# Performance work log

Hardware: AMD Instinct MI355X
Metric: run time of the kernel (lower is better)

Reference implementation:

```python
import jax, jax.numpy as jnp
import numpy as np

IMG_H, IMG_W = 512.0, 512.0
PRE_NMS = 2000   # training-mode pre_nms_top_n
POST_NMS = 2000  # training-mode post_nms_top_n
NMS_THRESH = 0.7
SCORE_THRESH = 0.0
MIN_SIZE = 0.001


def setup_inputs() -> dict:
    key = jax.random.key(0)
    k1, k2, k3 = jax.random.split(key, 3)
    N = 8
    num_anchors_per_level = (49152, 12288, 3072, 768, 192)  # strides 4..64, 3 anchors/loc on 512^2
    A = sum(num_anchors_per_level)
    cxy = jax.random.uniform(k1, (N, A, 2), minval=0.0, maxval=512.0)
    wh = jax.random.uniform(k2, (N, A, 2), minval=2.0, maxval=120.0)
    proposals = jnp.concatenate([cxy - wh / 2, cxy + wh / 2], axis=-1)  # xyxy
    objectness = jax.random.normal(k3, (N, A), dtype=jnp.float32)
    return {"proposals": proposals, "objectness": objectness,
            "num_anchors_per_level": num_anchors_per_level}


def _box_iou(a, b):
    # a: [K,4], b: [K,4] -> [K,K] pairwise IoU (torchvision box_iou semantics)
    area_a = (a[:, 2] - a[:, 0]) * (a[:, 3] - a[:, 1])
    area_b = (b[:, 2] - b[:, 0]) * (b[:, 3] - b[:, 1])
    lt = jnp.maximum(a[:, None, :2], b[None, :, :2])
    rb = jnp.minimum(a[:, None, 2:], b[None, :, 2:])
    wh = jnp.clip(rb - lt, 0.0)
    inter = wh[..., 0] * wh[..., 1]
    return inter / (area_a[:, None] + area_b[None, :] - inter)


def _per_image(boxes, scores, lvl):
    # boxes [K,4] xyxy, scores [K] (sigmoid probs), lvl [K] int32 level ids
    # 1) clip to image
    x = jnp.clip(boxes[:, 0::2], 0.0, IMG_W)
    y = jnp.clip(boxes[:, 1::2], 0.0, IMG_H)
    boxes = jnp.stack([x[:, 0], y[:, 0], x[:, 1], y[:, 1]], axis=-1)
    # 2) small-box + 3) score-threshold masks (masking instead of boolean indexing)
    ws = boxes[:, 2] - boxes[:, 0]
    hs = boxes[:, 3] - boxes[:, 1]
    valid = (ws >= MIN_SIZE) & (hs >= MIN_SIZE) & (scores >= SCORE_THRESH)
    # 4) batched NMS: offset boxes per level so levels never overlap
    off = lvl.astype(boxes.dtype) * (jnp.max(boxes) + 1.0)
    off_boxes = boxes + off[:, None]
    sm = jnp.where(valid, scores, -jnp.inf)
    order = jnp.argsort(-sm)                 # descending score, invalid last
    boxes_s = boxes[order]
    scores_s = scores[order]
    valid_s = valid[order]
    ob_s = jax.lax.stop_gradient(off_boxes[order])
    K = ob_s.shape[0]
    iou = _box_iou(ob_s, ob_s)               # [K,K], keep decision is non-differentiable
    j = jnp.arange(K)
    def body(i, keep):
        suppress = keep[i] & (iou[i] > NMS_THRESH) & (j > i)
        return keep & ~suppress
    keep = jax.lax.fori_loop(0, K, body, valid_s)
    # 5) top post_nms kept boxes, padded to fixed size with zeros
    rank = jnp.cumsum(keep.astype(jnp.int32)) - 1
    sel_key = jnp.where(keep & (rank < POST_NMS), rank, K)
    idx = jnp.argsort(sel_key)[:POST_NMS]
    out_valid = sel_key[idx] < K
    out_boxes = jnp.where(out_valid[:, None], boxes_s[idx], 0.0)
    out_scores = jnp.where(out_valid, scores_s[idx], 0.0)
    return out_boxes, out_scores


def _forward(proposals, objectness, num_anchors_per_level):
    N = proposals.shape[0]
    napl = [int(n) for n in num_anchors_per_level]
    # per-level, per-image top-k on objectness (get_top_n_idx)
    idx_list, lv_list, off = [], [], 0
    for i, n in enumerate(napl):
        k = min(PRE_NMS, n)
        _, ti = jax.lax.top_k(objectness[:, off:off + n], k)
        idx_list.append(ti + off)
        lv_list.append(jnp.full((k,), i, dtype=jnp.int32))
        off += n
    top_idx = jnp.concatenate(idx_list, axis=1)   # [N, K_total]
    lvls = jnp.concatenate(lv_list)               # [K_total], same for every image
    bidx = jnp.arange(N)[:, None]
    obj = objectness[bidx, top_idx]
    props = proposals[bidx, top_idx]
    scores = jax.nn.sigmoid(obj)
    return jax.vmap(lambda b, s: _per_image(b, s, lvls))(props, scores)


def reference(proposals, objectness, num_anchors_per_level):
    # returns (boxes [N, POST_NMS, 4], scores [N, POST_NMS]); invalid slots zero-padded
    return _forward(proposals, objectness, num_anchors_per_level)
```

## Files before the change

kernel.cpp:

```cpp
#include <hip/hip_runtime.h>
#include <math.h>

#define NIMG 8
#define ATOT 65472
#define KTOT 6960
#define POST 2000
#define TILES_PER_IMG 1668
#define NTILES (NIMG*TILES_PER_IMG)
#define ESEG 1024
#define M_TIE 0.7000000178813934326171875
#define PAD(i) ((i) + ((i) >> 5))
#define WAVE_SYNC() asm volatile("s_waitcnt lgkmcnt(0)" ::: "memory")

__constant__ int c_NAPL[5]  = {49152,12288,3072,768,192};
__constant__ int c_LOFF[5]  = {0,49152,61440,64512,65280};
__constant__ int c_KSEL[5]  = {2000,2000,2000,768,192};
__constant__ int c_CBASE[5] = {0,2000,4000,6000,6768};
__constant__ int c_GLVL[5]  = {32,32,32,12,3};
__constant__ int c_TILEPFX[6] = {0,528,1056,1584,1662,1668};

__device__ __forceinline__ unsigned f2u(float f){
  unsigned b = __float_as_uint(f);
  return (b & 0x80000000u) ? ~b : (b | 0x80000000u);
}
__device__ __forceinline__ unsigned long long mkkey(unsigned u, unsigned gidx){
  return ((unsigned long long)u << 32) | (unsigned long long)(0xFFFFFFFFu - gidx);
}
__device__ __forceinline__ unsigned long long shflx64(unsigned long long v, int m){
  int lo = __shfl_xor((int)(unsigned)v, m);
  int hi = __shfl_xor((int)(unsigned)(v >> 32), m);
  return ((unsigned long long)(unsigned)hi << 32) | (unsigned)lo;
}
__device__ __forceinline__ unsigned long long bstep(unsigned long long v, int elem,
                                                    int size, int st){
  unsigned long long p = shflx64(v, st);
  bool lower = (elem & st) == 0;
  bool desc  = (elem & size) == 0;
  bool takeMax = (lower == desc);
  bool gt = v > p;
  return (takeMax == gt) ? v : p;
}

extern "C" __global__ void __launch_bounds__(1024)
k_select(const float* __restrict__ prop, const float* __restrict__ obj,
         unsigned long long* __restrict__ cand, float4* __restrict__ cbox,
         unsigned* __restrict__ zzone){
  __shared__ unsigned long long sb[2112];
  __shared__ unsigned hist[4096];
  __shared__ unsigned scan[1024];
  __shared__ unsigned h8[256];
  __shared__ unsigned s_b12, s_cumAbove, s_t20, s_cnt;
  int task = blockIdx.x, img = task/5, lvl = task%5;
  int n = c_NAPL[lvl], k = c_KSEL[lvl], tid = threadIdx.x;
  if (task == 0)
    for (int i = tid; i < 1280; i += 1024) zzone[i] = 0u;

  const float4* o4 = (const float4*)(obj + (size_t)img*ATOT + c_LOFF[lvl]);
  int n4 = n >> 2;
  unsigned kk = (unsigned)k;
  unsigned T = 0u;
  if (k < n){
    for (int i = tid; i < 4096; i += 1024) hist[i] = 0u;
    if (tid < 256) h8[tid] = 0u;
    __syncthreads();
    for (int i = tid; i < n4; i += 1024){
      float4 v = o4[i];
      atomicAdd(&hist[f2u(v.x) >> 20], 1u);
      atomicAdd(&hist[f2u(v.y) >> 20], 1u);
      atomicAdd(&hist[f2u(v.z) >> 20], 1u);
      atomicAdd(&hist[f2u(v.w) >> 20], 1u);
    }
    __syncthreads();
    unsigned own[4]; unsigned s = 0;
    int b0 = tid*4;
    #pragma unroll
    for (int j = 0; j < 4; ++j){ own[j] = hist[b0+j]; s += own[j]; }
    scan[tid] = s;
    __syncthreads();
    for (int d = 1; d < 1024; d <<= 1){
      unsigned v = (tid + d < 1024) ? scan[tid + d] : 0u;
      __syncthreads();
      scan[tid] += v;
      __syncthreads();
    }
    {
      unsigned R = scan[tid] - s;
      unsigned sufn = R;
      #pragma unroll
      for (int j = 3; j >= 0; --j){
        unsigned sufj = sufn + own[j];
        if (sufj >= kk && sufn < kk){ s_b12 = (unsigned)(b0 + j); s_cumAbove = sufn; }
        sufn = sufj;
      }
    }
    __syncthreads();
    unsigned b12 = s_b12;
    for (int i = tid; i < n4; i += 1024){
      float4 v = o4[i];
      unsigned ux = f2u(v.x), uy = f2u(v.y), uz = f2u(v.z), uw = f2u(v.w);
      if ((ux >> 20) == b12) atomicAdd(&h8[(ux >> 12) & 255u], 1u);
      if ((uy >> 20) == b12) atomicAdd(&h8[(uy >> 12) & 255u], 1u);
      if ((uz >> 20) == b12) atomicAdd(&h8[(uz >> 12) & 255u], 1u);
      if ((uw >> 20) == b12) atomicAdd(&h8[(uw >> 12) & 255u], 1u);
    }
    __syncthreads();
    if (tid < 256) scan[tid] = h8[tid];
    __syncthreads();
    for (int d = 1; d < 256; d <<= 1){
      unsigned v = 0;
      if (tid < 256) v = (tid + d < 256) ? scan[tid + d] : 0u;
      __syncthreads();
      if (tid < 256) scan[tid] += v;
      __syncthreads();
    }
    if (tid < 256){
      unsigned sufj = s_cumAbove + scan[tid];
      unsigned sufn = s_cumAbove + ((tid < 255) ? scan[tid + 1] : 0u);
      if (sufj >= kk && sufn < kk) s_t20 = (s_b12 << 8) | (unsigned)tid;
    }
    __syncthreads();
    T = s_t20;
  }
  if (tid == 0) s_cnt = 0u;
  __syncthreads();
  int abase = c_LOFF[lvl];
  int lane = tid & 63, wv = tid >> 6;
  for (int i = tid; i < n4; i += 1024){
    float4 v = o4[i];
    float vv[4] = {v.x, v.y, v.z, v.w};
    #pragma unroll
    for (int c2 = 0; c2 < 4; ++c2){
      unsigned u = f2u(vv[c2]);
      bool pred = (u >> 12) >= T;
      unsigned long long bm = __ballot(pred);
      unsigned cw = (unsigned)__popcll(bm);
      unsigned basep = 0;
      if (lane == 0 && cw) basep = atomicAdd(&s_cnt, cw);
      basep = __shfl(basep, 0);
      if (pred){
        unsigned p = basep + (unsigned)__popcll(bm & ((1ull << lane) - 1ull));
        if (p < 2048u) sb[PAD(p)] = mkkey(u, (unsigned)(abase + i*4 + c2));
      }
    }
  }
  __syncthreads();
  int cnt = (int)min(s_cnt, 2048u);
  int m = 256; while (m < k || m < cnt) m <<= 1;
  for (int i = cnt + tid; i < m; i += 1024) sb[PAD(i)] = 0ull;
  __syncthreads();

  int elemA = (wv << 7) | lane, elemB = elemA | 64;
  bool active = (elemA < m);
  unsigned long long va = 0ull, vb = 0ull;
  if (active){ va = sb[PAD(elemA)]; vb = sb[PAD(elemB)]; }
  if (active){
    for (int size = 2; size <= 64; size <<= 1)
      for (int st = size >> 1; st >= 1; st >>= 1){
        va = bstep(va, elemA, size, st);
        vb = bstep(vb, elemB, size, st);
      }
    {
      bool desc = ((elemA & 128) == 0);
      unsigned long long mx = (va > vb) ? va : vb;
      unsigned long long mn = (va > vb) ? vb : va;
      va = desc ? mx : mn; vb = desc ? mn : mx;
      for (int st = 32; st >= 1; st >>= 1){
        va = bstep(va, elemA, 128, st);
        vb = bstep(vb, elemB, 128, st);
      }
    }
  }
  for (int S = 256; S <= m; S <<= 1){
    if (active){ sb[PAD(elemA)] = va; sb[PAD(elemB)] = vb; }
    __syncthreads();
    for (int st = S >> 1; st >= 128; st >>= 1){
      for (int t = tid; t < (m >> 1); t += 1024){
        int lo = t & (st - 1);
        int i  = ((t - lo) << 1) + lo;
        int j  = i + st;
        bool desc = ((i & S) == 0);
        unsigned long long x = sb[PAD(i)], y = sb[PAD(j)];
        if (desc ? (x < y) : (x > y)){ sb[PAD(i)] = y; sb[PAD(j)] = x; }
      }
      __syncthreads();
    }
    if (active){
      va = sb[PAD(elemA)]; vb = sb[PAD(elemB)];
      bool desc = ((elemA & S) == 0);
      unsigned long long mx = (va > vb) ? va : vb;
      unsigned long long mn = (va > vb) ? vb : va;
      va = desc ? mx : mn; vb = desc ? mn : mx;
      for (int st = 32; st >= 1; st >>= 1){
        va = bstep(va, elemA, S, st);
        vb = bstep(vb, elemB, S, st);
      }
    }
  }
  const float4* pr = (const float4*)(prop + (size_t)img*ATOT*4);
  size_t base = (size_t)img*KTOT + c_CBASE[lvl];
  if (active){
    if (elemA < k){
      cand[base + elemA] = va;
      unsigned gidx = 0xFFFFFFFFu - (unsigned)(va & 0xFFFFFFFFull);
      float4 p = pr[gidx];
      cbox[base + elemA] = make_float4(fminf(fmaxf(p.x,0.f),512.f), fminf(fmaxf(p.y,0.f),512.f),
                                       fminf(fmaxf(p.z,0.f),512.f), fminf(fmaxf(p.w,0.f),512.f));
    }
    if (elemB < k){
      cand[base + elemB] = vb;
      unsigned gidx = 0xFFFFFFFFu - (unsigned)(vb & 0xFFFFFFFFull);
      float4 p = pr[gidx];
      cbox[base + elemB] = make_float4(fminf(fmaxf(p.x,0.f),512.f), fminf(fmaxf(p.y,0.f),512.f),
                                       fminf(fmaxf(p.z,0.f),512.f), fminf(fmaxf(p.w,0.f),512.f));
    }
  }
}

extern "C" __global__ void __launch_bounds__(256)
k_mask(const float4* __restrict__ cbox, unsigned* __restrict__ ecnt,
       unsigned* __restrict__ eseg, float4* __restrict__ out4, int out_n4){
  __shared__ float4 colb[4][64];
  __shared__ float  colA[4][64];
  int tid = threadIdx.x, lane = tid & 63, wv = tid >> 6;
  int bid = blockIdx.x;
  if (bid < 79){
    int z = bid*256 + tid;
    if (z < out_n4) out4[z] = make_float4(0.f,0.f,0.f,0.f);
  }
  int tile = bid*4 + wv;
  int img = tile / TILES_PER_IMG, r = tile % TILES_PER_IMG;
  int lvl = 0;
  while (r >= c_TILEPFX[lvl + 1]) ++lvl;
  int t = r - c_TILEPFX[lvl];
  int G = c_GLVL[lvl], k = c_KSEL[lvl];
  int gi = 0;
  while (t >= G - gi){ t -= G - gi; ++gi; }
  int gj = gi + t;
  int task = img*5 + lvl;
  const float4* cb = cbox + (size_t)img*KTOT + c_CBASE[lvl];

  int jj = gj*64 + lane;
  float4 bb = (jj < k) ? cb[jj] : make_float4(0.f,0.f,0.f,0.f);
  colb[wv][lane] = bb;
  colA[wv][lane] = (bb.z - bb.x) * (bb.w - bb.y);
  WAVE_SYNC();

  int i = gi*64 + lane;
  float4 a = cb[(i < k) ? i : (k - 1)];
  float aarea = (a.z - a.x) * (a.w - a.y);
  unsigned long long word = 0ull;
  #pragma unroll
  for (int j = 0; j < 64; ++j){
    float4 b = colb[wv][j];
    float bA = colA[wv][j];
    float ix = fminf(a.z, b.z) - fmaxf(a.x, b.x);
    float iy = fminf(a.w, b.w) - fmaxf(a.y, b.y);
    float inter = ix * iy;
    float uni = (aarea + bA) - inter;
    float p7 = 0.7f * uni;
    int d = __float_as_int(inter) - __float_as_int(p7);
    bool ov  = (ix > 0.f) & (iy > 0.f);
    bool hit = ov & (d > 8);
    bool amb = ov & (d > -9) & (d <= 8);
    if (__any(amb)){
      if (amb && ((double)inter >= M_TIE * (double)uni)) hit = true;
    }
    word |= hit ? (1ull << j) : 0ull;
  }
  if (i >= k) word = 0ull;
  if (gi == gj)
    word &= (lane == 63) ? 0ull : (~0ull << (lane + 1));

  int nb = __popcll(word);
  int pfx = nb;
  for (int d = 1; d < 64; d <<= 1){
    int v = __shfl_up(pfx, d);
    if (lane >= d) pfx += v;
  }
  int total = __shfl(pfx, 63);
  if (total > 0){
    unsigned base = 0;
    if (lane == 0) base = atomicAdd(&ecnt[task*32 + gi], (unsigned)total);
    base = __shfl(base, 0);
    unsigned idx = base + (unsigned)(pfx - nb);
    unsigned* ep = eseg + (size_t)(task*32 + gi)*ESEG;
    while (word){
      int j = __ffsll(word) - 1; word &= word - 1;
      if (idx < ESEG) ep[idx] = ((unsigned)i << 16) | (unsigned)(gj*64 + j);
      ++idx;
    }
  }
}

extern "C" __global__ void __launch_bounds__(256)
k_scan(const unsigned long long* __restrict__ cand, const unsigned* __restrict__ ecnt,
       const unsigned* __restrict__ eseg, unsigned long long* __restrict__ clist,
       unsigned* __restrict__ ccnt){
  __shared__ unsigned ledge[6144];
  __shared__ unsigned soff[33], wpfx[33];
  __shared__ unsigned long long sm[64];
  __shared__ unsigned long long remW[32], keepW[32];
  __shared__ unsigned long long s_hasI;
  int task = blockIdx.x, img = task / 5, lvl = task % 5;
  int k = c_KSEL[lvl], nW = c_GLVL[lvl], tid = threadIdx.x;

  if (tid == 0){
    unsigned s = 0;
    for (int w = 0; w < nW; ++w){ soff[w] = s; s += min(ecnt[task*32 + w], (unsigned)ESEG); }
    soff[nW] = s;
  }
  if (tid < 32) remW[tid] = 0ull;
  __syncthreads();
  for (int w = 0; w < nW; ++w){
    unsigned c = soff[w+1] - soff[w];
    const unsigned* ep = eseg + (size_t)(task*32 + w)*ESEG;
    for (unsigned e = tid; e < c; e += 256){
      unsigned p = soff[w] + e;
      if (p < 6144u) ledge[p] = ep[e];
    }
  }
  __syncthreads();

  if (tid < 64){
    int lane = tid;
    for (int w = 0; w < nW; ++w){
      unsigned c = soff[w+1] - soff[w];
      if (c == 0) continue;
      const unsigned* ep = eseg + (size_t)(task*32 + w)*ESEG;
      sm[lane] = 0ull;
      if (lane == 0) s_hasI = 0ull;
      WAVE_SYNC();
      for (unsigned e = lane; e < c; e += 64){
        unsigned p = soff[w] + e;
        unsigned ed = (p < 6144u) ? ledge[p] : ep[e];
        int i = (int)(ed >> 16), j = (int)(ed & 0xFFFFu);
        if ((j >> 6) == w){
          atomicOr(&sm[i & 63], 1ull << (j & 63));
          atomicOr(&s_hasI, 1ull << (i & 63));
        }
      }
      WAVE_SYNC();
      if (lane == 0){
        unsigned long long r = remW[w];
        unsigned long long x = s_hasI & ~r;
        while (x){
          int i = __ffsll(x) - 1;
          r |= sm[i];
          x &= ~(1ull << i);
          x &= ~r;
        }
        remW[w] = r;
      }
      WAVE_SYNC();
      unsigned long long keep_w = ~remW[w];
      for (unsigned e = lane; e < c; e += 64){
        unsigned p = soff[w] + e;
        unsigned ed = (p < 6144u) ? ledge[p] : ep[e];
        int i = (int)(ed >> 16), j = (int)(ed & 0xFFFFu), wj = j >> 6;
        if (wj != w && ((keep_w >> (i & 63)) & 1ull))
          atomicOr(&remW[wj], 1ull << (j & 63));
      }
      WAVE_SYNC();
    }
    if (lane < 32){
      unsigned long long v = 0ull;
      if (lane < nW){
        int rem = k - lane*64;
        v = (rem >= 64) ? ~0ull : ((1ull << rem) - 1ull);
      }
      keepW[lane] = v & ~remW[lane];
    }
    WAVE_SYNC();
    if (lane == 0){
      unsigned s = 0;
      for (int w = 0; w < nW; ++w){ wpfx[w] = s; s += (unsigned)__popcll(keepW[w]); }
      ccnt[task] = s;
    }
  }
  __syncthreads();
  size_t base = (size_t)img*KTOT + c_CBASE[lvl];
  for (int i = tid; i < k; i += 256){
    unsigned long long w = keepW[i >> 6];
    if ((w >> (i & 63)) & 1ull){
      unsigned long long lowmask = (i & 63) ? ((1ull << (i & 63)) - 1ull) : 0ull;
      unsigned rank = wpfx[i >> 6] + (unsigned)__popcll(w & lowmask);
      clist[base + rank] = cand[base + i];
    }
  }
}

__device__ __forceinline__ int cntGreater(const unsigned long long* base, int len,
                                          unsigned long long x){
  int lo = 0, hi = len;
  while (lo < hi){
    int mid = (lo + hi) >> 1;
    if (base[mid] > x) lo = mid + 1; else hi = mid;
  }
  return lo;
}

extern "C" __global__ void __launch_bounds__(1024)
k_merge(const float* __restrict__ prop, const float* __restrict__ obj,
        const unsigned long long* __restrict__ clist, const unsigned* __restrict__ ccnt,
        float* __restrict__ out){
  __shared__ unsigned long long keys[KTOT];
  __shared__ int loff[6], lcnt[5];
  int img = blockIdx.x >> 3, eighth = blockIdx.x & 7, tid = threadIdx.x;
  if (tid == 0){
    int s = 0;
    for (int l = 0; l < 5; ++l){ lcnt[l] = (int)ccnt[img*5 + l]; loff[l] = s; s += lcnt[l]; }
    loff[5] = s;
  }
  __syncthreads();
  for (int l = 0; l < 5; ++l){
    size_t gb = (size_t)img*KTOT + c_CBASE[l];
    int c = lcnt[l], lo = loff[l];
    for (int e = tid; e < c; e += 1024) keys[lo + e] = clist[gb + e];
  }
  __syncthreads();
  const float4* pr = (const float4*)(prop + (size_t)img*ATOT*4);
  const float*  o  = obj + (size_t)img*ATOT;
  float* ob = out + (size_t)img*POST*4;
  float* os = out + (size_t)NIMG*POST*4 + (size_t)img*POST;
  int tot = loff[5];
  for (int tt = tid; ; tt += 1024){
    int t = 8*tt + eighth;
    if (t >= tot) break;
    int lvl = 0;
    while (t >= loff[lvl + 1]) ++lvl;
    unsigned long long x = keys[t];
    int pos = t - loff[lvl];
    for (int l = 0; l < 5; ++l){
      if (l == lvl) continue;
      pos += cntGreater(keys + loff[l], lcnt[l], x);
    }
    if (pos < POST){
      unsigned gidx = 0xFFFFFFFFu - (unsigned)(x & 0xFFFFFFFFull);
      float4 p = pr[gidx];
      ob[pos*4 + 0] = fminf(fmaxf(p.x, 0.f), 512.f);
      ob[pos*4 + 1] = fminf(fmaxf(p.y, 0.f), 512.f);
      ob[pos*4 + 2] = fminf(fmaxf(p.z, 0.f), 512.f);
      ob[pos*4 + 3] = fminf(fmaxf(p.w, 0.f), 512.f);
      double sgm = 1.0 / (1.0 + exp(-(double)o[gidx]));
      os[pos] = (float)sgm;
    }
  }
}

extern "C" void kernel_launch(void* const* d_in, const int* in_sizes, int n_in,
                              void* d_out, int out_size, void* d_ws, size_t ws_size,
                              hipStream_t stream){
  const float* prop = (const float*)d_in[0];
  const float* obj  = (const float*)d_in[1];
  char* ws = (char*)d_ws;
  unsigned*           ecnt = (unsigned*)(ws);
  unsigned*           ccnt = (unsigned*)(ws + 5120);
  unsigned long long* cand = (unsigned long long*)(ws + 5632);
  unsigned long long* clist= (unsigned long long*)(ws + 451072);
  float4*             cbox = (float4*)(ws + 896512);
  unsigned*           eseg = (unsigned*)(ws + 1787392);

  int out_n4 = out_size / 4;
  hipLaunchKernelGGL(k_select, dim3(40),  dim3(1024), 0, stream, prop, obj, cand, cbox, ecnt);
  hipLaunchKernelGGL(k_mask,   dim3(NTILES/4), dim3(256), 0, stream, cbox, ecnt, eseg,
                     (float4*)d_out, out_n4);
  hipLaunchKernelGGL(k_scan,   dim3(40),  dim3(256),  0, stream, cand, ecnt, eseg, clist, ccnt);
  hipLaunchKernelGGL(k_merge,  dim3(64),  dim3(1024), 0, stream, prop, obj, clist, ccnt, (float*)d_out);
}
```

Before: 183.7 us.

## Fuse NMS scan into mask kernel via last-tile-done atomic trigger

```diff
diff --git a/kernel.cpp b/kernel.cpp
--- a/kernel.cpp
+++ b/kernel.cpp
@@ -18,6 +18,7 @@
 __constant__ int c_CBASE[5] = {0,2000,4000,6000,6768};
 __constant__ int c_GLVL[5]  = {32,32,32,12,3};
 __constant__ int c_TILEPFX[6] = {0,528,1056,1584,1662,1668};
+__constant__ int c_TTASK[5] = {528,528,528,78,6};
 
 __device__ __forceinline__ unsigned f2u(float f){
   unsigned b = __float_as_uint(f);
@@ -53,7 +54,7 @@
   int task = blockIdx.x, img = task/5, lvl = task%5;
   int n = c_NAPL[lvl], k = c_KSEL[lvl], tid = threadIdx.x;
   if (task == 0)
-    for (int i = tid; i < 1280; i += 1024) zzone[i] = 0u;
+    for (int i = tid; i < 1360; i += 1024) zzone[i] = 0u;
 
   const float4* o4 = (const float4*)(obj + (size_t)img*ATOT + c_LOFF[lvl]);
   int n4 = n >> 2;
@@ -216,11 +217,116 @@
   }
 }
 
+__device__ void run_scan(int task,
+    const unsigned long long* __restrict__ cand, const unsigned* __restrict__ ecnt,
+    const unsigned* __restrict__ eseg, unsigned long long* __restrict__ clist,
+    unsigned* __restrict__ ccnt,
+    unsigned* ledge, unsigned* soff, unsigned* wpfx,
+    unsigned long long* sm, unsigned long long* remW, unsigned long long* keepW,
+    unsigned long long* s_hasI){
+  int img = task / 5, lvl = task % 5;
+  int k = c_KSEL[lvl], nW = c_GLVL[lvl], tid = threadIdx.x;
+
+  if (tid == 0){
+    unsigned s = 0;
+    for (int w = 0; w < nW; ++w){ soff[w] = s; s += min(ecnt[task*32 + w], (unsigned)ESEG); }
+    soff[nW] = s;
+  }
+  if (tid < 32) remW[tid] = 0ull;
+  __syncthreads();
+  for (int w = 0; w < nW; ++w){
+    unsigned c = soff[w+1] - soff[w];
+    const unsigned* ep = eseg + (size_t)(task*32 + w)*ESEG;
+    for (unsigned e = tid; e < c; e += 256){
+      unsigned p = soff[w] + e;
+      if (p < 6144u) ledge[p] = ep[e];
+    }
+  }
+  __syncthreads();
+
+  if (tid < 64){
+    int lane = tid;
+    for (int w = 0; w < nW; ++w){
+      unsigned c = soff[w+1] - soff[w];
+      if (c == 0) continue;
+      const unsigned* ep = eseg + (size_t)(task*32 + w)*ESEG;
+      sm[lane] = 0ull;
+      if (lane == 0) *s_hasI = 0ull;
+      WAVE_SYNC();
+      for (unsigned e = lane; e < c; e += 64){
+        unsigned p = soff[w] + e;
+        unsigned ed = (p < 6144u) ? ledge[p] : ep[e];
+        int i = (int)(ed >> 16), j = (int)(ed & 0xFFFFu);
+        if ((j >> 6) == w){
+          atomicOr(&sm[i & 63], 1ull << (j & 63));
+          atomicOr(s_hasI, 1ull << (i & 63));
+        }
+      }
+      WAVE_SYNC();
+      if (lane == 0){
+        unsigned long long r = remW[w];
+        unsigned long long x = *s_hasI & ~r;
+        while (x){
+          int i = __ffsll(x) - 1;
+          r |= sm[i];
+          x &= ~(1ull << i);
+          x &= ~r;
+        }
+        remW[w] = r;
+      }
+      WAVE_SYNC();
+      unsigned long long keep_w = ~remW[w];
+      for (unsigned e = lane; e < c; e += 64){
+        unsigned p = soff[w] + e;
+        unsigned ed = (p < 6144u) ? ledge[p] : ep[e];
+        int i = (int)(ed >> 16), j = (int)(ed & 0xFFFFu), wj = j >> 6;
+        if (wj != w && ((keep_w >> (i & 63)) & 1ull))
+          atomicOr(&remW[wj], 1ull << (j & 63));
+      }
+      WAVE_SYNC();
+    }
+    if (lane < 32){
+      unsigned long long v = 0ull;
+      if (lane < nW){
+        int rem = k - lane*64;
+        v = (rem >= 64) ? ~0ull : ((1ull << rem) - 1ull);
+      }
+      keepW[lane] = v & ~remW[lane];
+    }
+    WAVE_SYNC();
+    if (lane == 0){
+      unsigned s = 0;
+      for (int w = 0; w < nW; ++w){ wpfx[w] = s; s += (unsigned)__popcll(keepW[w]); }
+      ccnt[task] = s;
+    }
+  }
+  __syncthreads();
+  size_t base = (size_t)img*KTOT + c_CBASE[lvl];
+  for (int i = tid; i < k; i += 256){
+    unsigned long long w = keepW[i >> 6];
+    if ((w >> (i & 63)) & 1ull){
+      unsigned long long lowmask = (i & 63) ? ((1ull << (i & 63)) - 1ull) : 0ull;
+      unsigned rank = wpfx[i >> 6] + (unsigned)__popcll(w & lowmask);
+      clist[base + rank] = cand[base + i];
+    }
+  }
+  __syncthreads();
+}
+
 extern "C" __global__ void __launch_bounds__(256)
 k_mask(const float4* __restrict__ cbox, unsigned* __restrict__ ecnt,
-       unsigned* __restrict__ eseg, float4* __restrict__ out4, int out_n4){
+       unsigned* __restrict__ eseg, float4* __restrict__ out4, int out_n4,
+       const unsigned long long* __restrict__ cand,
+       unsigned long long* __restrict__ clist, unsigned* __restrict__ ccnt,
+       unsigned* __restrict__ tdone){
   __shared__ float4 colb[4][64];
   __shared__ float  colA[4][64];
+  __shared__ int    s_trig[4];
+  __shared__ unsigned ledge[6144];
+  __shared__ unsigned soff[33], wpfx[33];
+  __shared__ unsigned long long sm[64];
+  __shared__ unsigned long long remW[32], keepW[32];
+  __shared__ unsigned long long s_hasI;
   int tid = threadIdx.x, lane = tid & 63, wv = tid >> 6;
   int bid = blockIdx.x;
   if (bid < 79){
@@ -290,101 +396,20 @@
       ++idx;
     }
   }
-}
-
-extern "C" __global__ void __launch_bounds__(256)
-k_scan(const unsigned long long* __restrict__ cand, const unsigned* __restrict__ ecnt,
-       const unsigned* __restrict__ eseg, unsigned long long* __restrict__ clist,
-       unsigned* __restrict__ ccnt){
-  __shared__ unsigned ledge[6144];
-  __shared__ unsigned soff[33], wpfx[33];
-  __shared__ unsigned long long sm[64];
-  __shared__ unsigned long long remW[32], keepW[32];
-  __shared__ unsigned long long s_hasI;
-  int task = blockIdx.x, img = task / 5, lvl = task % 5;
-  int k = c_KSEL[lvl], nW = c_GLVL[lvl], tid = threadIdx.x;
-
-  if (tid == 0){
-    unsigned s = 0;
-    for (int w = 0; w < nW; ++w){ soff[w] = s; s += min(ecnt[task*32 + w], (unsigned)ESEG); }
-    soff[nW] = s;
-  }
-  if (tid < 32) remW[tid] = 0ull;
-  __syncthreads();
-  for (int w = 0; w < nW; ++w){
-    unsigned c = soff[w+1] - soff[w];
-    const unsigned* ep = eseg + (size_t)(task*32 + w)*ESEG;
-    for (unsigned e = tid; e < c; e += 256){
-      unsigned p = soff[w] + e;
-      if (p < 6144u) ledge[p] = ep[e];
-    }
-  }
-  __syncthreads();
-
-  if (tid < 64){
-    int lane = tid;
-    for (int w = 0; w < nW; ++w){
-      unsigned c = soff[w+1] - soff[w];
-      if (c == 0) continue;
-      const unsigned* ep = eseg + (size_t)(task*32 + w)*ESEG;
-      sm[lane] = 0ull;
-      if (lane == 0) s_hasI = 0ull;
-      WAVE_SYNC();
-      for (unsigned e = lane; e < c; e += 64){
-        unsigned p = soff[w] + e;
-        unsigned ed = (p < 6144u) ? ledge[p] : ep[e];
-        int i = (int)(ed >> 16), j = (int)(ed & 0xFFFFu);
-        if ((j >> 6) == w){
-          atomicOr(&sm[i & 63], 1ull << (j & 63));
-          atomicOr(&s_hasI, 1ull << (i & 63));
-        }
-      }
-      WAVE_SYNC();
-      if (lane == 0){
-        unsigned long long r = remW[w];
-        unsigned long long x = s_hasI & ~r;
-        while (x){
-          int i = __ffsll(x) - 1;
-          r |= sm[i];
-          x &= ~(1ull << i);
-          x &= ~r;
-        }
-        remW[w] = r;
-      }
-      WAVE_SYNC();
-      unsigned long long keep_w = ~remW[w];
-      for (unsigned e = lane; e < c; e += 64){
-        unsigned p = soff[w] + e;
-        unsigned ed = (p < 6144u) ? ledge[p] : ep[e];
-        int i = (int)(ed >> 16), j = (int)(ed & 0xFFFFu), wj = j >> 6;
-        if (wj != w && ((keep_w >> (i & 63)) & 1ull))
-          atomicOr(&remW[wj], 1ull << (j & 63));
-      }
-      WAVE_SYNC();
-    }
-    if (lane < 32){
-      unsigned long long v = 0ull;
-      if (lane < nW){
-        int rem = k - lane*64;
-        v = (rem >= 64) ? ~0ull : ((1ull << rem) - 1ull);
-      }
-      keepW[lane] = v & ~remW[lane];
-    }
-    WAVE_SYNC();
-    if (lane == 0){
-      unsigned s = 0;
-      for (int w = 0; w < nW; ++w){ wpfx[w] = s; s += (unsigned)__popcll(keepW[w]); }
-      ccnt[task] = s;
-    }
-  }
-  __syncthreads();
-  size_t base = (size_t)img*KTOT + c_CBASE[lvl];
-  for (int i = tid; i < k; i += 256){
-    unsigned long long w = keepW[i >> 6];
-    if ((w >> (i & 63)) & 1ull){
-      unsigned long long lowmask = (i & 63) ? ((1ull << (i & 63)) - 1ull) : 0ull;
-      unsigned rank = wpfx[i >> 6] + (unsigned)__popcll(w & lowmask);
-      clist[base + rank] = cand[base + i];
+
+  __threadfence();
+  if (lane == 0){
+    unsigned done = atomicAdd(&tdone[task], 1u);
+    s_trig[wv] = (done == (unsigned)(c_TTASK[lvl] - 1)) ? task : -1;
+  }
+  __syncthreads();
+  #pragma unroll
+  for (int q = 0; q < 4; ++q){
+    int st = s_trig[q];
+    if (st >= 0){
+      __threadfence();
+      run_scan(st, cand, ecnt, eseg, clist, ccnt,
+               ledge, soff, wpfx, sm, remW, keepW, &s_hasI);
     }
   }
 }
@@ -455,6 +480,7 @@
   char* ws = (char*)d_ws;
   unsigned*           ecnt = (unsigned*)(ws);
   unsigned*           ccnt = (unsigned*)(ws + 5120);
+  unsigned*           tdone= (unsigned*)(ws + 5280);
   unsigned long long* cand = (unsigned long long*)(ws + 5632);
   unsigned long long* clist= (unsigned long long*)(ws + 451072);
   float4*             cbox = (float4*)(ws + 896512);
@@ -463,7 +489,6 @@
   int out_n4 = out_size / 4;
   hipLaunchKernelGGL(k_select, dim3(40),  dim3(1024), 0, stream, prop, obj, cand, cbox, ecnt);
   hipLaunchKernelGGL(k_mask,   dim3(NTILES/4), dim3(256), 0, stream, cbox, ecnt, eseg,
-                     (float4*)d_out, out_n4);
-  hipLaunchKernelGGL(k_scan,   dim3(40),  dim3(256),  0, stream, cand, ecnt, eseg, clist, ccnt);
+                     (float4*)d_out, out_n4, cand, clist, ccnt, tdone);
   hipLaunchKernelGGL(k_merge,  dim3(64),  dim3(1024), 0, stream, prop, obj, clist, ccnt, (float*)d_out);
 }
```

Result: slower. 372.3 us (+102.7%).
